# Performance work log

Measured on AMD Instinct MI355X. Metric: run time of the kernel, lower is better.

## Reference

```python
import jax, jax.numpy as jnp
import numpy as np

D_MODEL = 1024
NEG_BIG = -1e9  # matches TF float32 branch


def setup_inputs() -> dict:
    key = jax.random.key(0)
    kq, kk, kv, km = jax.random.split(key, 4)
    B, S, D = 4, 2048, D_MODEL
    q = jax.random.normal(kq, (B, S, D), dtype=jnp.float32)
    k = jax.random.normal(kk, (B, S, D), dtype=jnp.float32)
    v = jax.random.normal(kv, (B, S, D), dtype=jnp.float32)
    mask = jax.random.randint(km, (B, 1, S), 0, 2, dtype=jnp.int32)  # 1 = masked
    return {"q": q, "k": k, "v": v, "mask": mask}


def reference(q, k, v, mask):
    scale = jnp.asarray(D_MODEL, q.dtype) ** -0.5
    # [B,S,S] attention logits
    logits = jnp.einsum("bqd,bkd->bqk", q, k) * scale
    logits = logits + mask.astype(q.dtype) * NEG_BIG
    weights = jax.nn.softmax(logits, axis=-1)
    return jnp.einsum("bqk,bkd->bqd", weights, v)
```

## Files before the change

kernel.cpp:

```cpp
#include <hip/hip_runtime.h>
#include <cstdint>

#define B_    4
#define S_    2048
#define D_    1024
#define SCALE 0.03125f
#define NEG_BIG -1e9f

typedef __attribute__((ext_vector_type(8))) short short8;
typedef __attribute__((ext_vector_type(4))) float f32x4;

__device__ __forceinline__ ushort f2bf(float f) {
  uint32_t u = __float_as_uint(f);
  u += 0x7fffu + ((u >> 16) & 1u);
  return (ushort)(u >> 16);
}

__device__ __forceinline__ void load16_to_lds(const void* g, void* l) {
  __builtin_amdgcn_global_load_lds(
      (const __attribute__((address_space(1))) uint32_t*)g,
      (__attribute__((address_space(3))) uint32_t*)l, 16, 0, 0);
}

__global__ void prep(const float* __restrict__ Q, const float* __restrict__ K,
                     const float* __restrict__ V, ushort* __restrict__ Qb,
                     ushort* __restrict__ Kb, ushort* __restrict__ Vt) {
  __shared__ ushort tile[64][68];
  int id = blockIdx.x;
  if (id < 8192) {
    const float* X = (id < 4096) ? Q : K;
    ushort* Xb     = (id < 4096) ? Qb : Kb;
    int cid = id & 4095;
    size_t i = ((size_t)cid * 256 + threadIdx.x) * 8;
    float4 a = *(const float4*)(X + i);
    float4 c = *(const float4*)(X + i + 4);
    uint4 w;
    w.x = (uint)f2bf(a.x) | ((uint)f2bf(a.y) << 16);
    w.y = (uint)f2bf(a.z) | ((uint)f2bf(a.w) << 16);
    w.z = (uint)f2bf(c.x) | ((uint)f2bf(c.y) << 16);
    w.w = (uint)f2bf(c.z) | ((uint)f2bf(c.w) << 16);
    *(uint4*)(Xb + i) = w;
    return;
  }
  int t = id - 8192;
  int s0 = (t & 31) * 64, d0 = ((t >> 5) & 15) * 64, b = t >> 9;
  int tx = threadIdx.x & 15, ty = threadIdx.x >> 4;
  const float* src = V + ((size_t)b * S_ + s0) * D_ + d0;
  for (int i = 0; i < 4; ++i) {
    int row = ty + i * 16;
    float4 a = *(const float4*)(src + (size_t)row * D_ + tx * 4);
    ushort4 w;
    w.x = f2bf(a.x); w.y = f2bf(a.y); w.z = f2bf(a.z); w.w = f2bf(a.w);
    *(ushort4*)&tile[row][tx * 4] = w;
  }
  __syncthreads();
  ushort* dst = Vt + ((size_t)b * D_ + d0) * S_ + s0;
  for (int i = 0; i < 4; ++i) {
    int drow = ty + i * 16;
    ushort4 w;
    w.x = tile[tx * 4 + 0][drow];
    w.y = tile[tx * 4 + 1][drow];
    w.z = tile[tx * 4 + 2][drow];
    w.w = tile[tx * 4 + 3][drow];
    *(ushort4*)(dst + (size_t)drow * S_ + tx * 4) = w;
  }
}

template<int KDIM, int LDA, int LDB, int LDC,
         long long BATCHA, long long BATCHB, long long BATCHC,
         int NBN, int EPI, typename OutT>
__global__ __launch_bounds__(512, 2)
void gemm2(const ushort* __restrict__ A, const ushort* __restrict__ Bt,
           OutT* __restrict__ C, const int* __restrict__ mask) {
  constexpr int SLOT = (256 + 128) * 64;
  constexpr int BOFF = 256 * 64;
  constexpr int NT   = KDIM / 64;
  __shared__ __align__(16) ushort lds[3 * SLOT];

  const int per = gridDim.x >> 3;
  int g = (blockIdx.x & 7) * per + (blockIdx.x >> 3);
  constexpr int TPB = 8 * NBN;
  int b  = g / TPB;
  int t0 = g % TPB;
  int bm = t0 / NBN;
  int sn = t0 % NBN;
  int bn = (bm & 1) ? (NBN - 1 - sn) : sn;

  int tid  = threadIdx.x;
  int lane = tid & 63;
  int wave = tid >> 6;
  int wr = wave >> 1, wc = wave & 1;
  int l16 = lane & 15, quad = lane >> 4;

  const ushort* Ab = A  + (size_t)b * BATCHA + (size_t)(bm * 256) * LDA;
  const ushort* Bb = Bt + (size_t)b * BATCHB + (size_t)(bn * 128) * LDB;

  float madd[4];
  if (EPI == 0) {
#pragma unroll
    for (int nt = 0; nt < 4; ++nt)
      madd[nt] = mask[b * S_ + bn * 128 + wc * 64 + nt * 16 + l16] ? NEG_BIG : 0.f;
  }

  f32x4 acc[4][4];
#pragma unroll
  for (int i = 0; i < 4; ++i)
#pragma unroll
    for (int j = 0; j < 4; ++j) acc[i][j] = (f32x4){0.f, 0.f, 0.f, 0.f};

  auto stage = [&](int kt, int slot) {
#pragma unroll
    for (int j = 0; j < 4; ++j) {
      int c = tid + j * 512;
      int row  = c >> 3;
      int col8 = (c & 7) * 8;
      int src8 = col8 ^ ((row & 7) << 3);
      load16_to_lds(Ab + (size_t)row * LDA + (size_t)kt * 64 + src8,
                    lds + slot * SLOT + c * 8);
    }
#pragma unroll
    for (int j = 0; j < 2; ++j) {
      int c = tid + j * 512;
      int row  = c >> 3;
      int col8 = (c & 7) * 8;
      int src8 = col8 ^ ((row & 7) << 3);
      load16_to_lds(Bb + (size_t)row * LDB + (size_t)kt * 64 + src8,
                    lds + slot * SLOT + BOFF + c * 8);
    }
  };

  stage(0, 0);
  stage(1, 1);
  asm volatile("s_waitcnt vmcnt(6)\n"
               "s_barrier" ::: "memory");

  int sc = 0;
  for (int t = 0; t < NT; ++t) {
    int s2 = sc + 2; if (s2 >= 3) s2 -= 3;
    if (t + 2 < NT) stage(t + 2, s2);

    const ushort* La = lds + sc * SLOT;
    const ushort* Lb = lds + sc * SLOT + BOFF;

    short8 a0[2][2], bfr[4][2];
#pragma unroll
    for (int ks = 0; ks < 2; ++ks) {
#pragma unroll
      for (int mt = 0; mt < 2; ++mt) {
        int row  = wr * 64 + mt * 16 + l16;
        int col8 = (ks * 32 + quad * 8) ^ ((row & 7) << 3);
        a0[mt][ks] = *(const short8*)(La + row * 64 + col8);
      }
#pragma unroll
      for (int nt = 0; nt < 4; ++nt) {
        int row  = wc * 64 + nt * 16 + l16;
        int col8 = (ks * 32 + quad * 8) ^ ((row & 7) << 3);
        bfr[nt][ks] = *(const short8*)(Lb + row * 64 + col8);
      }
    }
    __builtin_amdgcn_s_setprio(1);
#pragma unroll
    for (int ks = 0; ks < 2; ++ks)
#pragma unroll
      for (int mt = 0; mt < 2; ++mt)
#pragma unroll
        for (int nt = 0; nt < 4; ++nt)
          acc[mt][nt] = __builtin_amdgcn_mfma_f32_16x16x32_bf16(
              a0[mt][ks], bfr[nt][ks], acc[mt][nt], 0, 0, 0);
    __builtin_amdgcn_s_setprio(0);
    asm volatile("s_barrier" ::: "memory");

    short8 a1[2][2];
#pragma unroll
    for (int ks = 0; ks < 2; ++ks)
#pragma unroll
      for (int mt = 0; mt < 2; ++mt) {
        int row  = wr * 64 + (mt + 2) * 16 + l16;
        int col8 = (ks * 32 + quad * 8) ^ ((row & 7) << 3);
        a1[mt][ks] = *(const short8*)(La + row * 64 + col8);
      }
    __builtin_amdgcn_s_setprio(1);
#pragma unroll
    for (int ks = 0; ks < 2; ++ks)
#pragma unroll
      for (int mt = 0; mt < 2; ++mt)
#pragma unroll
        for (int nt = 0; nt < 4; ++nt)
          acc[mt + 2][nt] = __builtin_amdgcn_mfma_f32_16x16x32_bf16(
              a1[mt][ks], bfr[nt][ks], acc[mt + 2][nt], 0, 0, 0);
    __builtin_amdgcn_s_setprio(0);

    if (t < NT - 3)
      asm volatile("s_waitcnt lgkmcnt(0)\n"
                   "s_waitcnt vmcnt(6)\n"
                   "s_barrier" ::: "memory");
    else
      asm volatile("s_waitcnt lgkmcnt(0)\n"
                   "s_waitcnt vmcnt(0)\n"
                   "s_barrier" ::: "memory");
    sc = (sc == 2) ? 0 : sc + 1;
  }

  OutT* Cb = C + (size_t)b * BATCHC + (size_t)(bm * 256) * LDC + (size_t)(bn * 128);
#pragma unroll
  for (int nt = 0; nt < 4; ++nt) {
    int col = wc * 64 + nt * 16 + l16;
#pragma unroll
    for (int mt = 0; mt < 4; ++mt)
#pragma unroll
      for (int r = 0; r < 4; ++r) {
        int row = wr * 64 + mt * 16 + quad * 4 + r;
        float v = acc[mt][nt][r];
        if (EPI == 0)
          Cb[(size_t)row * LDC + col] = (OutT)f2bf(v * SCALE + madd[nt]);
        else
          Cb[(size_t)row * LDC + col] = (OutT)v;
      }
  }
}

__global__ void softmax_rows(const ushort* __restrict__ S, ushort* __restrict__ P) {
  int row = blockIdx.x * 4 + (threadIdx.x >> 6);
  int lane = threadIdx.x & 63;
  const ushort* src = S + (size_t)row * S_;

  float x[32];
#pragma unroll
  for (int j = 0; j < 4; ++j) {
    uint4 v = *(const uint4*)(src + lane * 8 + j * 512);
    uint32_t w[4] = {v.x, v.y, v.z, v.w};
#pragma unroll
    for (int t = 0; t < 4; ++t) {
      x[j * 8 + t * 2 + 0] = __uint_as_float(w[t] << 16);
      x[j * 8 + t * 2 + 1] = __uint_as_float(w[t] & 0xffff0000u);
    }
  }
  float m = x[0];
#pragma unroll
  for (int i = 1; i < 32; ++i) m = fmaxf(m, x[i]);
  for (int off = 1; off < 64; off <<= 1) m = fmaxf(m, __shfl_xor(m, off));

  float e[32], s = 0.f;
#pragma unroll
  for (int i = 0; i < 32; ++i) { e[i] = __expf(x[i] - m); s += e[i]; }
  for (int off = 1; off < 64; off <<= 1) s += __shfl_xor(s, off);
  float rinv = 1.0f / s;

  ushort* dst = P + (size_t)row * S_;
#pragma unroll
  for (int j = 0; j < 4; ++j) {
    uint4 w;
    uint32_t* pw = &w.x;
#pragma unroll
    for (int t = 0; t < 4; ++t)
      pw[t] = (uint32_t)f2bf(e[j * 8 + t * 2] * rinv) |
              ((uint32_t)f2bf(e[j * 8 + t * 2 + 1] * rinv) << 16);
    *(uint4*)(dst + lane * 8 + j * 512) = w;
  }
}

extern "C" void kernel_launch(void* const* d_in, const int* in_sizes, int n_in,
                              void* d_out, int out_size, void* d_ws, size_t ws_size,
                              hipStream_t stream) {
  const float* Q   = (const float*)d_in[0];
  const float* K   = (const float*)d_in[1];
  const float* V   = (const float*)d_in[2];
  const int*  mask = (const int*)d_in[3];
  float* Out = (float*)d_out;

  const size_t E = (size_t)B_ * S_ * D_;
  ushort* Qb = (ushort*)d_ws;
  ushort* Kb = Qb + E;
  ushort* Vt = Kb + E;
  ushort* Sb = Vt + E;
  ushort* P  = Qb;

  prep<<<10240, 256, 0, stream>>>(Q, K, V, Qb, Kb, Vt);

  gemm2<1024, 1024, 1024, 2048,
        (long long)2048 * 1024, (long long)2048 * 1024, (long long)2048 * 2048,
        16, 0, ushort>
      <<<512, 512, 0, stream>>>(Qb, Kb, Sb, mask);

  softmax_rows<<<2048, 256, 0, stream>>>(Sb, P);

  gemm2<2048, 2048, 2048, 1024,
        (long long)2048 * 2048, (long long)1024 * 2048, (long long)2048 * 1024,
        8, 1, float>
      <<<256, 512, 0, stream>>>(P, Vt, Out, nullptr);
}
```

Measured before the change: 229.6 us.

## Split GEMM into specialized QK and PV kernels with double-buffered interleaved staging

Replaces the shared templated GEMM with two specialized kernels. The QK^T kernel now uses 256x256 tiles (256 blocks) with a 2x4 wave layout, and both kernels move from triple- to double-buffered LDS. Global-to-LDS staging is split into halves and interleaved between four or two MFMA phases per k-step, with barriers and lgkmcnt waits in between. The goal is more reuse per tile in QK and better overlap of loads with MFMA. The costs are more barriers per iteration, higher register pressure from 8x4 accumulators, and fewer blocks in the QK grid.

Measured after the change: 225.7 us. No clear change (-1.7%).

```diff
diff --git a/kernel.cpp b/kernel.cpp
--- a/kernel.cpp
+++ b/kernel.cpp
@@ -21,6 +21,11 @@
       (const __attribute__((address_space(1))) uint32_t*)g,
       (__attribute__((address_space(3))) uint32_t*)l, 16, 0, 0);
 }
+
+#define BAR()   __builtin_amdgcn_s_barrier()
+#define LGKM0() do { asm volatile("s_waitcnt lgkmcnt(0)" ::: "memory"); \
+                     __builtin_amdgcn_sched_barrier(0); } while (0)
+#define VM(n)   asm volatile("s_waitcnt vmcnt(" #n ")" ::: "memory")
 
 __global__ void prep(const float* __restrict__ Q, const float* __restrict__ K,
                      const float* __restrict__ V, ushort* __restrict__ Qb,
@@ -66,41 +71,197 @@
   }
 }
 
-template<int KDIM, int LDA, int LDB, int LDC,
-         long long BATCHA, long long BATCHB, long long BATCHC,
-         int NBN, int EPI, typename OutT>
 __global__ __launch_bounds__(512, 2)
-void gemm2(const ushort* __restrict__ A, const ushort* __restrict__ Bt,
-           OutT* __restrict__ C, const int* __restrict__ mask) {
-  constexpr int SLOT = (256 + 128) * 64;
-  constexpr int BOFF = 256 * 64;
-  constexpr int NT   = KDIM / 64;
-  __shared__ __align__(16) ushort lds[3 * SLOT];
+void gemm_qk(const ushort* __restrict__ A, const ushort* __restrict__ Bt,
+             ushort* __restrict__ C, const int* __restrict__ mask) {
+  constexpr int NT  = 1024 / 64;
+  constexpr int BUF = 512 * 64;
+  constexpr int BO  = 256 * 64;
+  __shared__ __align__(16) ushort lds[2 * BUF];
 
   const int per = gridDim.x >> 3;
-  int g = (blockIdx.x & 7) * per + (blockIdx.x >> 3);
-  constexpr int TPB = 8 * NBN;
-  int b  = g / TPB;
-  int t0 = g % TPB;
-  int bm = t0 / NBN;
-  int sn = t0 % NBN;
-  int bn = (bm & 1) ? (NBN - 1 - sn) : sn;
-
-  int tid  = threadIdx.x;
-  int lane = tid & 63;
-  int wave = tid >> 6;
+  int g  = (blockIdx.x & 7) * per + (blockIdx.x >> 3);
+  int b  = g >> 6;
+  int t0 = g & 63;
+  int bm = t0 >> 3;
+  int sn = t0 & 7;
+  int bn = (bm & 1) ? 7 - sn : sn;
+
+  int tid = threadIdx.x, lane = tid & 63, wave = tid >> 6;
+  int wr = wave >> 2, wc = wave & 3;
+  int l16 = lane & 15, quad = lane >> 4;
+
+  const ushort* Ab = A  + (size_t)b * (2048LL * 1024) + (size_t)(bm * 256) * 1024;
+  const ushort* Bb = Bt + (size_t)b * (2048LL * 1024) + (size_t)(bn * 256) * 1024;
+
+  float madd[4];
+#pragma unroll
+  for (int nt = 0; nt < 4; ++nt)
+    madd[nt] = mask[b * S_ + bn * 256 + wc * 64 + nt * 16 + l16] ? NEG_BIG : 0.f;
+
+  f32x4 acc[8][4];
+#pragma unroll
+  for (int i = 0; i < 8; ++i)
+#pragma unroll
+    for (int j = 0; j < 4; ++j) acc[i][j] = (f32x4){0.f, 0.f, 0.f, 0.f};
+
+  auto stageA = [&](int kt, int half) {
+#pragma unroll
+    for (int j = 0; j < 2; ++j) {
+      int c = tid + j * 512;
+      int row = half * 128 + (c >> 3);
+      int col = ((c & 7) * 8) ^ ((row & 7) << 3);
+      load16_to_lds(Ab + (size_t)row * 1024 + kt * 64 + col,
+                    lds + (size_t)(kt & 1) * BUF + (half * 1024 + c) * 8);
+    }
+  };
+  auto stageB = [&](int kt, int half) {
+#pragma unroll
+    for (int j = 0; j < 2; ++j) {
+      int c = tid + j * 512;
+      int row = half * 128 + (c >> 3);
+      int col = ((c & 7) * 8) ^ ((row & 7) << 3);
+      load16_to_lds(Bb + (size_t)row * 1024 + kt * 64 + col,
+                    lds + (size_t)(kt & 1) * BUF + BO + (half * 1024 + c) * 8);
+    }
+  };
+
+  stageA(0, 0); stageA(0, 1); stageB(0, 0); stageB(0, 1);
+  stageB(1, 0); stageB(1, 1);
+  VM(4);
+  BAR();
+
+  for (int t = 0; t < NT; ++t) {
+    const ushort* La = lds + (size_t)(t & 1) * BUF;
+    const ushort* Lb = La + BO;
+    short8 a0[4][2], a1[4][2], b0[2][2], b1[2][2];
+
+    if (t + 1 < NT) stageA(t + 1, 0);
+#pragma unroll
+    for (int mt = 0; mt < 4; ++mt)
+#pragma unroll
+      for (int ks = 0; ks < 2; ++ks) {
+        int row = wr * 128 + mt * 16 + l16;
+        a0[mt][ks] = *(const short8*)(La + row * 64 + ((ks * 32 + quad * 8) ^ ((row & 7) << 3)));
+      }
+#pragma unroll
+    for (int nt = 0; nt < 2; ++nt)
+#pragma unroll
+      for (int ks = 0; ks < 2; ++ks) {
+        int row = wc * 64 + nt * 16 + l16;
+        b0[nt][ks] = *(const short8*)(Lb + row * 64 + ((ks * 32 + quad * 8) ^ ((row & 7) << 3)));
+      }
+    BAR(); LGKM0();
+    __builtin_amdgcn_s_setprio(1);
+#pragma unroll
+    for (int ks = 0; ks < 2; ++ks)
+#pragma unroll
+      for (int mt = 0; mt < 4; ++mt)
+#pragma unroll
+        for (int nt = 0; nt < 2; ++nt)
+          acc[mt][nt] = __builtin_amdgcn_mfma_f32_16x16x32_bf16(
+              a0[mt][ks], b0[nt][ks], acc[mt][nt], 0, 0, 0);
+    __builtin_amdgcn_s_setprio(0);
+    BAR();
+
+    if (t + 1 < NT) stageA(t + 1, 1);
+#pragma unroll
+    for (int nt = 0; nt < 2; ++nt)
+#pragma unroll
+      for (int ks = 0; ks < 2; ++ks) {
+        int row = wc * 64 + (nt + 2) * 16 + l16;
+        b1[nt][ks] = *(const short8*)(Lb + row * 64 + ((ks * 32 + quad * 8) ^ ((row & 7) << 3)));
+      }
+#pragma unroll
+    for (int mt = 0; mt < 4; ++mt) {
+      int row = wr * 128 + (mt + 4) * 16 + l16;
+      a1[mt][0] = *(const short8*)(La + row * 64 + ((quad * 8) ^ ((row & 7) << 3)));
+    }
+    BAR(); LGKM0();
+    __builtin_amdgcn_s_setprio(1);
+#pragma unroll
+    for (int ks = 0; ks < 2; ++ks)
+#pragma unroll
+      for (int mt = 0; mt < 4; ++mt)
+#pragma unroll
+        for (int nt = 0; nt < 2; ++nt)
+          acc[mt][nt + 2] = __builtin_amdgcn_mfma_f32_16x16x32_bf16(
+              a0[mt][ks], b1[nt][ks], acc[mt][nt + 2], 0, 0, 0);
+    __builtin_amdgcn_s_setprio(0);
+    BAR();
+
+    if (t + 2 < NT) stageB(t + 2, 0);
+#pragma unroll
+    for (int mt = 0; mt < 4; ++mt) {
+      int row = wr * 128 + (mt + 4) * 16 + l16;
+      a1[mt][1] = *(const short8*)(La + row * 64 + ((32 + quad * 8) ^ ((row & 7) << 3)));
+    }
+    BAR(); LGKM0();
+    __builtin_amdgcn_s_setprio(1);
+#pragma unroll
+    for (int ks = 0; ks < 2; ++ks)
+#pragma unroll
+      for (int mt = 0; mt < 4; ++mt)
+#pragma unroll
+        for (int nt = 0; nt < 2; ++nt)
+          acc[mt + 4][nt + 2] = __builtin_amdgcn_mfma_f32_16x16x32_bf16(
+              a1[mt][ks], b1[nt][ks], acc[mt + 4][nt + 2], 0, 0, 0);
+    __builtin_amdgcn_s_setprio(0);
+    BAR();
+
+    if (t + 2 < NT) stageB(t + 2, 1);
+    __builtin_amdgcn_s_setprio(1);
+#pragma unroll
+    for (int ks = 0; ks < 2; ++ks)
+#pragma unroll
+      for (int mt = 0; mt < 4; ++mt)
+#pragma unroll
+        for (int nt = 0; nt < 2; ++nt)
+          acc[mt + 4][nt] = __builtin_amdgcn_mfma_f32_16x16x32_bf16(
+              a1[mt][ks], b0[nt][ks], acc[mt + 4][nt], 0, 0, 0);
+    __builtin_amdgcn_s_setprio(0);
+
+    if (t < NT - 2)      VM(4);
+    else if (t == NT - 2) VM(0);
+    BAR();
+  }
+
+  ushort* Cb = C + (size_t)b * (2048LL * 2048) + (size_t)(bm * 256) * 2048 + bn * 256;
+#pragma unroll
+  for (int nt = 0; nt < 4; ++nt) {
+    int col = wc * 64 + nt * 16 + l16;
+#pragma unroll
+    for (int mt = 0; mt < 8; ++mt)
+#pragma unroll
+      for (int r = 0; r < 4; ++r) {
+        int row = wr * 128 + mt * 16 + quad * 4 + r;
+        Cb[(size_t)row * 2048 + col] = f2bf(acc[mt][nt][r] * SCALE + madd[nt]);
+      }
+  }
+}
+
+__global__ __launch_bounds__(512, 2)
+void gemm_pv(const ushort* __restrict__ A, const ushort* __restrict__ Bt,
+             float* __restrict__ C) {
+  constexpr int NT  = 2048 / 64;
+  constexpr int BUF = (256 + 128) * 64;
+  constexpr int BO  = 256 * 64;
+  __shared__ __align__(16) ushort lds[2 * BUF];
+
+  const int per = gridDim.x >> 3;
+  int g  = (blockIdx.x & 7) * per + (blockIdx.x >> 3);
+  int b  = g >> 6;
+  int t0 = g & 63;
+  int bm = t0 >> 3;
+  int sn = t0 & 7;
+  int bn = (bm & 1) ? 7 - sn : sn;
+
+  int tid = threadIdx.x, lane = tid & 63, wave = tid >> 6;
   int wr = wave >> 1, wc = wave & 1;
   int l16 = lane & 15, quad = lane >> 4;
 
-  const ushort* Ab = A  + (size_t)b * BATCHA + (size_t)(bm * 256) * LDA;
-  const ushort* Bb = Bt + (size_t)b * BATCHB + (size_t)(bn * 128) * LDB;
-
-  float madd[4];
-  if (EPI == 0) {
-#pragma unroll
-    for (int nt = 0; nt < 4; ++nt)
-      madd[nt] = mask[b * S_ + bn * 128 + wc * 64 + nt * 16 + l16] ? NEG_BIG : 0.f;
-  }
+  const ushort* Ab = A  + (size_t)b * (2048LL * 2048) + (size_t)(bm * 256) * 2048;
+  const ushort* Bb = Bt + (size_t)b * (1024LL * 2048) + (size_t)(bn * 128) * 2048;
 
   f32x4 acc[4][4];
 #pragma unroll
@@ -108,100 +269,91 @@
 #pragma unroll
     for (int j = 0; j < 4; ++j) acc[i][j] = (f32x4){0.f, 0.f, 0.f, 0.f};
 
-  auto stage = [&](int kt, int slot) {
-#pragma unroll
-    for (int j = 0; j < 4; ++j) {
-      int c = tid + j * 512;
-      int row  = c >> 3;
-      int col8 = (c & 7) * 8;
-      int src8 = col8 ^ ((row & 7) << 3);
-      load16_to_lds(Ab + (size_t)row * LDA + (size_t)kt * 64 + src8,
-                    lds + slot * SLOT + c * 8);
-    }
+  auto stageA = [&](int kt, int half) {
 #pragma unroll
     for (int j = 0; j < 2; ++j) {
       int c = tid + j * 512;
-      int row  = c >> 3;
-      int col8 = (c & 7) * 8;
-      int src8 = col8 ^ ((row & 7) << 3);
-      load16_to_lds(Bb + (size_t)row * LDB + (size_t)kt * 64 + src8,
-                    lds + slot * SLOT + BOFF + c * 8);
+      int row = half * 128 + (c >> 3);
+      int col = ((c & 7) * 8) ^ ((row & 7) << 3);
+      load16_to_lds(Ab + (size_t)row * 2048 + kt * 64 + col,
+                    lds + (size_t)(kt & 1) * BUF + (half * 1024 + c) * 8);
     }
   };
-
-  stage(0, 0);
-  stage(1, 1);
-  asm volatile("s_waitcnt vmcnt(6)\n"
-               "s_barrier" ::: "memory");
-
-  int sc = 0;
+  auto stageB = [&](int kt) {
+#pragma unroll
+    for (int j = 0; j < 2; ++j) {
+      int c = tid + j * 512;
+      int row = c >> 3;
+      int col = ((c & 7) * 8) ^ ((row & 7) << 3);
+      load16_to_lds(Bb + (size_t)row * 2048 + kt * 64 + col,
+                    lds + (size_t)(kt & 1) * BUF + BO + c * 8);
+    }
+  };
+
+  stageA(0, 0); stageA(0, 1); stageB(0);
+  stageA(1, 0); stageA(1, 1);
+  VM(4);
+  BAR();
+
   for (int t = 0; t < NT; ++t) {
-    int s2 = sc + 2; if (s2 >= 3) s2 -= 3;
-    if (t + 2 < NT) stage(t + 2, s2);
-
-    const ushort* La = lds + sc * SLOT;
-    const ushort* Lb = lds + sc * SLOT + BOFF;
-
-    short8 a0[2][2], bfr[4][2];
-#pragma unroll
-    for (int ks = 0; ks < 2; ++ks) {
-#pragma unroll
-      for (int mt = 0; mt < 2; ++mt) {
-        int row  = wr * 64 + mt * 16 + l16;
-        int col8 = (ks * 32 + quad * 8) ^ ((row & 7) << 3);
-        a0[mt][ks] = *(const short8*)(La + row * 64 + col8);
-      }
-#pragma unroll
-      for (int nt = 0; nt < 4; ++nt) {
-        int row  = wc * 64 + nt * 16 + l16;
-        int col8 = (ks * 32 + quad * 8) ^ ((row & 7) << 3);
-        bfr[nt][ks] = *(const short8*)(Lb + row * 64 + col8);
-      }
-    }
-    __builtin_amdgcn_s_setprio(1);
-#pragma unroll
-    for (int ks = 0; ks < 2; ++ks)
-#pragma unroll
-      for (int mt = 0; mt < 2; ++mt)
-#pragma unroll
-        for (int nt = 0; nt < 4; ++nt)
+    const ushort* La = lds + (size_t)(t & 1) * BUF;
+    const ushort* Lb = La + BO;
+    short8 a[4][2], b0[2][2], b1[2][2];
+
+    if (t + 1 < NT) stageB(t + 1);
+#pragma unroll
+    for (int mt = 0; mt < 4; ++mt)
+#pragma unroll
+      for (int ks = 0; ks < 2; ++ks) {
+        int row = wr * 64 + mt * 16 + l16;
+        a[mt][ks] = *(const short8*)(La + row * 64 + ((ks * 32 + quad * 8) ^ ((row & 7) << 3)));
+      }
+#pragma unroll
+    for (int nt = 0; nt < 2; ++nt)
+#pragma unroll
+      for (int ks = 0; ks < 2; ++ks) {
+        int row = wc * 64 + nt * 16 + l16;
+        b0[nt][ks] = *(const short8*)(Lb + row * 64 + ((ks * 32 + quad * 8) ^ ((row & 7) << 3)));
+      }
+    BAR(); LGKM0();
+    __builtin_amdgcn_s_setprio(1);
+#pragma unroll
+    for (int ks = 0; ks < 2; ++ks)
+#pragma unroll
+      for (int mt = 0; mt < 4; ++mt)
+#pragma unroll
+        for (int nt = 0; nt < 2; ++nt)
           acc[mt][nt] = __builtin_amdgcn_mfma_f32_16x16x32_bf16(
-              a0[mt][ks], bfr[nt][ks], acc[mt][nt], 0, 0, 0);
-    __builtin_amdgcn_s_setprio(0);
-    asm volatile("s_barrier" ::: "memory");
-
-    short8 a1[2][2];
-#pragma unroll
-    for (int ks = 0; ks < 2; ++ks)
-#pragma unroll
-      for (int mt = 0; mt < 2; ++mt) {
-        int row  = wr * 64 + (mt + 2) * 16 + l16;
-        int col8 = (ks * 32 + quad * 8) ^ ((row & 7) << 3);
-        a1[mt][ks] = *(const short8*)(La + row * 64 + col8);
-      }
-    __builtin_amdgcn_s_setprio(1);
-#pragma unroll
-    for (int ks = 0; ks < 2; ++ks)
-#pragma unroll
-      for (int mt = 0; mt < 2; ++mt)
-#pragma unroll
-        for (int nt = 0; nt < 4; ++nt)
-          acc[mt + 2][nt] = __builtin_amdgcn_mfma_f32_16x16x32_bf16(
-              a1[mt][ks], bfr[nt][ks], acc[mt + 2][nt], 0, 0, 0);
-    __builtin_amdgcn_s_setprio(0);
-
-    if (t < NT - 3)
-      asm volatile("s_waitcnt lgkmcnt(0)\n"
-                   "s_waitcnt vmcnt(6)\n"
-                   "s_barrier" ::: "memory");
-    else
-      asm volatile("s_waitcnt lgkmcnt(0)\n"
-                   "s_waitcnt vmcnt(0)\n"
-                   "s_barrier" ::: "memory");
-    sc = (sc == 2) ? 0 : sc + 1;
-  }
-
-  OutT* Cb = C + (size_t)b * BATCHC + (size_t)(bm * 256) * LDC + (size_t)(bn * 128);
+              a[mt][ks], b0[nt][ks], acc[mt][nt], 0, 0, 0);
+    __builtin_amdgcn_s_setprio(0);
+    BAR();
+
+    if (t + 2 < NT) { stageA(t + 2, 0); stageA(t + 2, 1); }
+#pragma unroll
+    for (int nt = 0; nt < 2; ++nt)
+#pragma unroll
+      for (int ks = 0; ks < 2; ++ks) {
+        int row = wc * 64 + (nt + 2) * 16 + l16;
+        b1[nt][ks] = *(const short8*)(Lb + row * 64 + ((ks * 32 + quad * 8) ^ ((row & 7) << 3)));
+      }
+    BAR(); LGKM0();
+    __builtin_amdgcn_s_setprio(1);
+#pragma unroll
+    for (int ks = 0; ks < 2; ++ks)
+#pragma unroll
+      for (int mt = 0; mt < 4; ++mt)
+#pragma unroll
+        for (int nt = 0; nt < 2; ++nt)
+          acc[mt][nt + 2] = __builtin_amdgcn_mfma_f32_16x16x32_bf16(
+              a[mt][ks], b1[nt][ks], acc[mt][nt + 2], 0, 0, 0);
+    __builtin_amdgcn_s_setprio(0);
+
+    if (t < NT - 2)      VM(4);
+    else if (t == NT - 2) VM(0);
+    BAR();
+  }
+
+  float* Cb = C + (size_t)b * (2048LL * 1024) + (size_t)(bm * 256) * 1024 + bn * 128;
 #pragma unroll
   for (int nt = 0; nt < 4; ++nt) {
     int col = wc * 64 + nt * 16 + l16;
@@ -210,11 +362,7 @@
 #pragma unroll
       for (int r = 0; r < 4; ++r) {
         int row = wr * 64 + mt * 16 + quad * 4 + r;
-        float v = acc[mt][nt][r];
-        if (EPI == 0)
-          Cb[(size_t)row * LDC + col] = (OutT)f2bf(v * SCALE + madd[nt]);
-        else
-          Cb[(size_t)row * LDC + col] = (OutT)v;
+        Cb[(size_t)row * 1024 + col] = acc[mt][nt][r];
       }
   }
 }
@@ -277,15 +425,9 @@
 
   prep<<<10240, 256, 0, stream>>>(Q, K, V, Qb, Kb, Vt);
 
-  gemm2<1024, 1024, 1024, 2048,
-        (long long)2048 * 1024, (long long)2048 * 1024, (long long)2048 * 2048,
-        16, 0, ushort>
-      <<<512, 512, 0, stream>>>(Qb, Kb, Sb, mask);
+  gemm_qk<<<256, 512, 0, stream>>>(Qb, Kb, Sb, mask);
 
   softmax_rows<<<2048, 256, 0, stream>>>(Sb, P);
 
-  gemm2<2048, 2048, 2048, 1024,
-        (long long)2048 * 2048, (long long)1024 * 2048, (long long)2048 * 1024,
-        8, 1, float>
-      <<<256, 512, 0, stream>>>(P, Vt, Out, nullptr);
-}
+  gemm_pv<<<256, 512, 0, stream>>>(P, Vt, Out);
+}
```
